# Kernel tuning notes

Measured on AMD Instinct MI355X. Metric: run time of the kernel, lower is better.

The kernel has to match this reference:

```python
import jax, jax.numpy as jnp
import numpy as np

WEIGHT = 0.1
TEMPERATURE = 0.07
EPS_NORM = 1e-12   # F.normalize eps
EPS_DEN = 1e-6     # denominator eps in pos_mask.sum()


def setup_inputs() -> dict:
    key = jax.random.key(0)
    k1, k2 = jax.random.split(key)
    features = jax.random.normal(k1, (4, 1000, 2048), dtype=jnp.float32)
    target = jax.random.randint(k2, (4, 1000), 0, 16, dtype=jnp.int64)
    return {"features": features, "target": target}


def _per_sample_loss(f, t):
    # f: [N, C], t: [N]
    N = f.shape[0]
    # F.normalize(dim=1)
    norm = jnp.maximum(jnp.linalg.norm(f, axis=1, keepdims=True), EPS_NORM)
    f = f / norm
    # [N, N] cosine similarities scaled by temperature
    sim = jnp.matmul(f, f.T) / TEMPERATURE
    eye = jnp.eye(N, dtype=f.dtype)
    pos = (t[:, None] == t[None, :]).astype(f.dtype) * (1.0 - eye)
    neg = 1.0 - pos - eye
    pos_sim = sim * pos
    # -log(exp(pos_sim) / (exp(pos_sim) + sum_j exp(sim)*neg))  summed over ALL entries
    denom = jnp.exp(pos_sim) + jnp.sum(jnp.exp(sim) * neg, axis=1, keepdims=True)
    loss_mat = jnp.log(denom) - pos_sim
    pos_sum = pos.sum()
    return loss_mat.sum() / (pos_sum + EPS_DEN), pos_sum


def reference(features, target):
    # features: [B, N, C] (already 3-D: no subsampling / interpolation paths fire)
    losses, pos_sums = jax.vmap(_per_sample_loss)(features, target)
    valid = pos_sums > 0
    num_pairs = valid.sum().astype(features.dtype)
    total = jnp.where(valid, losses, 0.0).sum()
    return jnp.where(num_pairs > 0, WEIGHT * total / num_pairs,
                     jnp.asarray(WEIGHT * 0.1, dtype=features.dtype))
```

## Files before the change

### kernel.cpp

```cpp
#include <hip/hip_runtime.h>
#include <math.h>

#define BB 4
#define NN 1000
#define NP 1024
#define CC 2048
#define TINV (1.0f / 0.07f)
#define BK 64

#define FNORM_BYTES ((size_t)BB * NP * CC * 2)
#define SIMP_BYTES  ((size_t)2 * BB * NP * NP * 4)
#define RL_BYTES    ((size_t)BB * NP * 4)

typedef __bf16 bf16x8 __attribute__((ext_vector_type(8)));
typedef float  f32x4  __attribute__((ext_vector_type(4)));
typedef float  f32x16 __attribute__((ext_vector_type(16)));

__device__ __forceinline__ void load_lds16(const void* g, void* l) {
    __builtin_amdgcn_global_load_lds(
        (const __attribute__((address_space(1))) unsigned int*)g,
        (__attribute__((address_space(3))) unsigned int*)l, 16, 0, 0);
}

__device__ __forceinline__ float blk_sum(float v, volatile float* lds) {
    int lane = threadIdx.x & 63;
    int wid  = threadIdx.x >> 6;
#pragma unroll
    for (int off = 32; off; off >>= 1) v += __shfl_down(v, off);
    __syncthreads();
    if (lane == 0) lds[wid] = v;
    __syncthreads();
    return lds[0] + lds[1] + lds[2] + lds[3];
}

__device__ __forceinline__ float wave_sum(float v) {
#pragma unroll
    for (int off = 32; off; off >>= 1) v += __shfl_down(v, off);
    return __shfl(v, 0);
}

__global__ __launch_bounds__(256) void norm_bf16_kernel(const float* __restrict__ f,
                                                        __bf16* __restrict__ out) {
    __shared__ float lds[4];
    __shared__ float scale_s;
    const int blk = blockIdx.x;
    const int b = blk >> 10, r = blk & (NP - 1);
    __bf16* dst = out + ((size_t)b * NP + r) * CC;
    const int tid = threadIdx.x;

    if (r >= NN) {
        ((uint4*)dst)[tid] = make_uint4(0u, 0u, 0u, 0u);
        return;
    }
    const float* src = f + ((size_t)b * NN + r) * CC;

    float ss = 0.f;
#pragma unroll
    for (int h = 0; h < 2; ++h) {
        float4 v = ((const float4*)src)[tid + h * 256];
        ss += v.x * v.x + v.y * v.y + v.z * v.z + v.w * v.w;
    }
    float tot = blk_sum(ss, lds);
    if (tid == 0) scale_s = 1.0f / fmaxf(sqrtf(tot), 1e-12f);
    __syncthreads();
    const float sc = scale_s;

    float4 v0 = ((const float4*)src)[tid * 2];
    float4 v1 = ((const float4*)src)[tid * 2 + 1];
    bf16x8 o;
    o[0] = (__bf16)(v0.x * sc); o[1] = (__bf16)(v0.y * sc);
    o[2] = (__bf16)(v0.z * sc); o[3] = (__bf16)(v0.w * sc);
    o[4] = (__bf16)(v1.x * sc); o[5] = (__bf16)(v1.y * sc);
    o[6] = (__bf16)(v1.z * sc); o[7] = (__bf16)(v1.w * sc);
    *(bf16x8*)(dst + tid * 8) = o;
}

__global__ __launch_bounds__(256) void simgemm_mfma(const __bf16* __restrict__ fn,
                                                    float* __restrict__ simp) {
    __shared__ __bf16 As[128 * BK];
    __shared__ __bf16 Bs[128 * BK];

    const int bz = blockIdx.z;
    const int b  = bz >> 1;
    const int kbeg = (bz & 1) * (CC / 2);
    const int tI = blockIdx.y * 128;
    const int tJ = blockIdx.x * 128;
    const __bf16* base = fn + (size_t)b * NP * CC;
    float* S = simp + (size_t)bz * NP * NP;

    const int tid  = threadIdx.x;
    const int wid  = tid >> 6;
    const int lane = tid & 63;
    const int wm   = wid >> 1;
    const int wn   = wid & 1;
    const int ln32 = lane & 31;
    const int kh   = lane >> 5;
    const int sw   = ln32 & 7;

    const int srow   = tid >> 3;
    const int schunk = (tid & 7) ^ (srow & 7);
    const __bf16* gA = base + (size_t)(tI + srow) * CC + kbeg + schunk * 8;
    const __bf16* gB = base + (size_t)(tJ + srow) * CC + kbeg + schunk * 8;
    __bf16* lA = As + (size_t)wid * 8 * BK;
    __bf16* lB = Bs + (size_t)wid * 8 * BK;

    f32x16 acc[2][2] = {};

    for (int k0 = 0; k0 < CC / 2; k0 += BK) {
#pragma unroll
        for (int r = 0; r < 4; ++r)
            load_lds16(gA + k0 + (size_t)r * 32 * CC, lA + r * 32 * BK);
#pragma unroll
        for (int r = 0; r < 4; ++r)
            load_lds16(gB + k0 + (size_t)r * 32 * CC, lB + r * 32 * BK);
        __syncthreads();

#pragma unroll
        for (int kc = 0; kc < 4; ++kc) {
            const int c = kc * 2 + kh;
            const int co = (c ^ sw) * 8;
            bf16x8 a0 = *(const bf16x8*)&As[(wm * 64      + ln32) * BK + co];
            bf16x8 a1 = *(const bf16x8*)&As[(wm * 64 + 32 + ln32) * BK + co];
            bf16x8 b0 = *(const bf16x8*)&Bs[(wn * 64      + ln32) * BK + co];
            bf16x8 b1 = *(const bf16x8*)&Bs[(wn * 64 + 32 + ln32) * BK + co];
            acc[0][0] = __builtin_amdgcn_mfma_f32_32x32x16_bf16(a0, b0, acc[0][0], 0, 0, 0);
            acc[0][1] = __builtin_amdgcn_mfma_f32_32x32x16_bf16(a0, b1, acc[0][1], 0, 0, 0);
            acc[1][0] = __builtin_amdgcn_mfma_f32_32x32x16_bf16(a1, b0, acc[1][0], 0, 0, 0);
            acc[1][1] = __builtin_amdgcn_mfma_f32_32x32x16_bf16(a1, b1, acc[1][1], 0, 0, 0);
        }
        __syncthreads();
    }

#pragma unroll
    for (int at = 0; at < 2; ++at) {
#pragma unroll
        for (int bt = 0; bt < 2; ++bt) {
            const int col = tJ + wn * 64 + bt * 32 + ln32;
#pragma unroll
            for (int r = 0; r < 16; ++r) {
                const int row = tI + wm * 64 + at * 32 + (r & 3) + 8 * (r >> 2) + 4 * kh;
                S[(size_t)row * NP + col] = acc[at][bt][r] * TINV;
            }
        }
    }
}

__global__ __launch_bounds__(256) void rowloss_kernel(const float* __restrict__ simp,
                                                      const int* __restrict__ tgt,
                                                      float* __restrict__ rloss,
                                                      float* __restrict__ rpos) {
    __shared__ int ts[NN];
    __shared__ float rowv[4][NP];
    const int b = blockIdx.y;
    const int wid = threadIdx.x >> 6, lane = threadIdx.x & 63;
    const int* t = tgt + (size_t)b * NN;
    for (int j = threadIdx.x; j < NN; j += 256) ts[j] = t[j];
    __syncthreads();

    const int i = blockIdx.x * 4 + wid;
    const float* r0 = simp + (size_t)(2 * b) * NP * NP + (size_t)i * NP;
    const float* r1 = r0 + (size_t)NP * NP;
    const int ti = ts[i];

    float sneg = 0.f, pcnt = 0.f;
    for (int g = lane; g < NN / 4; g += 64) {
        float4 a = ((const float4*)r0)[g];
        float4 c = ((const float4*)r1)[g];
        float4 v = make_float4(a.x + c.x, a.y + c.y, a.z + c.z, a.w + c.w);
        *(float4*)&rowv[wid][g * 4] = v;
        int4 tj = *(const int4*)&ts[g * 4];
        const int j = g * 4;
        if (j + 0 != i) { if (tj.x == ti) pcnt += 1.f; else sneg += __expf(v.x); }
        if (j + 1 != i) { if (tj.y == ti) pcnt += 1.f; else sneg += __expf(v.y); }
        if (j + 2 != i) { if (tj.z == ti) pcnt += 1.f; else sneg += __expf(v.z); }
        if (j + 3 != i) { if (tj.w == ti) pcnt += 1.f; else sneg += __expf(v.w); }
    }
    const float Sv = wave_sum(sneg);
    const float p  = wave_sum(pcnt);

    float term = 0.f;
    for (int g = lane; g < NN / 4; g += 64) {
        float4 v = *(const float4*)&rowv[wid][g * 4];
        int4 tj = *(const int4*)&ts[g * 4];
        const int j = g * 4;
        if (j + 0 != i && tj.x == ti) term += __logf(__expf(v.x) + Sv) - v.x;
        if (j + 1 != i && tj.y == ti) term += __logf(__expf(v.y) + Sv) - v.y;
        if (j + 2 != i && tj.z == ti) term += __logf(__expf(v.z) + Sv) - v.z;
        if (j + 3 != i && tj.w == ti) term += __logf(__expf(v.w) + Sv) - v.w;
    }
    const float tt = wave_sum(term);
    if (lane == 0) {
        rloss[b * NP + i] = tt + ((float)NN - p) * __logf(1.f + Sv);
        rpos [b * NP + i] = p;
    }
}

__global__ __launch_bounds__(256) void final_kernel(const float* __restrict__ rloss,
                                                    const float* __restrict__ rpos,
                                                    float* __restrict__ out) {
    __shared__ float lds[4];
    float total = 0.f, np = 0.f;
    for (int b = 0; b < BB; ++b) {
        float l = 0.f, p = 0.f;
        for (int i = threadIdx.x; i < NN; i += 256) {
            l += rloss[b * NP + i];
            p += rpos [b * NP + i];
        }
        float ls = blk_sum(l, lds);
        float ps = blk_sum(p, lds);
        if (ps > 0.f) { total += ls / (ps + 1e-6f); np += 1.f; }
    }
    if (threadIdx.x == 0)
        out[0] = (np > 0.f) ? 0.1f * total / np : 0.1f * 0.1f;
}

extern "C" void kernel_launch(void* const* d_in, const int* in_sizes, int n_in,
                              void* d_out, int out_size, void* d_ws, size_t ws_size,
                              hipStream_t stream) {
    const float* feat = (const float*)d_in[0];
    const int*   tgt  = (const int*)d_in[1];
    __bf16* fnorm = (__bf16*)d_ws;
    float*  simp  = (float*)((char*)d_ws + FNORM_BYTES);
    float*  rloss = (float*)((char*)d_ws + FNORM_BYTES + SIMP_BYTES);
    float*  rpos  = (float*)((char*)d_ws + FNORM_BYTES + SIMP_BYTES + RL_BYTES);

    norm_bf16_kernel<<<dim3(BB * NP), 256, 0, stream>>>(feat, fnorm);
    simgemm_mfma<<<dim3(NP / 128, NP / 128, 2 * BB), 256, 0, stream>>>(fnorm, simp);
    rowloss_kernel<<<dim3(NN / 4, BB), 256, 0, stream>>>(simp, tgt, rloss, rpos);
    final_kernel<<<1, 256, 0, stream>>>(rloss, rpos, (float*)d_out);
}
```

Before: 120.5 us.

## Store split-K similarity partials in bf16 and double-buffer GEMM LDS tiles

The split-K similarity partials are now written and read as bf16 instead of fp32. This halves the global-memory traffic between the GEMM and the row-loss kernel, and the row-loss loop now loads 8 bf16 values per lane. The GEMM main loop also gets two LDS buffers, so the next K-tile's global-to-LDS loads are issued before the current tile is computed. The cost is precision: scaled similarities can reach about 14, and rounding each partial to bf16 before exponentiation may push the loss past tolerance.

After: 116.1 us. 1.04x faster.

```diff
diff --git a/kernel.cpp b/kernel.cpp
--- a/kernel.cpp
+++ b/kernel.cpp
@@ -9,7 +9,7 @@
 #define BK 64
 
 #define FNORM_BYTES ((size_t)BB * NP * CC * 2)
-#define SIMP_BYTES  ((size_t)2 * BB * NP * NP * 4)
+#define SIMB_BYTES  ((size_t)2 * BB * NP * NP * 2)
 #define RL_BYTES    ((size_t)BB * NP * 4)
 
 typedef __bf16 bf16x8 __attribute__((ext_vector_type(8)));
@@ -76,9 +76,9 @@
 }
 
 __global__ __launch_bounds__(256) void simgemm_mfma(const __bf16* __restrict__ fn,
-                                                    float* __restrict__ simp) {
-    __shared__ __bf16 As[128 * BK];
-    __shared__ __bf16 Bs[128 * BK];
+                                                    __bf16* __restrict__ simb) {
+    __shared__ __bf16 As0[128 * BK], As1[128 * BK];
+    __shared__ __bf16 Bs0[128 * BK], Bs1[128 * BK];
 
     const int bz = blockIdx.z;
     const int b  = bz >> 1;
@@ -86,7 +86,7 @@
     const int tI = blockIdx.y * 128;
     const int tJ = blockIdx.x * 128;
     const __bf16* base = fn + (size_t)b * NP * CC;
-    float* S = simp + (size_t)bz * NP * NP;
+    __bf16* S = simb + (size_t)bz * NP * NP;
 
     const int tid  = threadIdx.x;
     const int wid  = tid >> 6;
@@ -101,35 +101,48 @@
     const int schunk = (tid & 7) ^ (srow & 7);
     const __bf16* gA = base + (size_t)(tI + srow) * CC + kbeg + schunk * 8;
     const __bf16* gB = base + (size_t)(tJ + srow) * CC + kbeg + schunk * 8;
-    __bf16* lA = As + (size_t)wid * 8 * BK;
-    __bf16* lB = Bs + (size_t)wid * 8 * BK;
+    const int wvoff = wid * 8 * BK;
 
     f32x16 acc[2][2] = {};
 
-    for (int k0 = 0; k0 < CC / 2; k0 += BK) {
-#pragma unroll
-        for (int r = 0; r < 4; ++r)
-            load_lds16(gA + k0 + (size_t)r * 32 * CC, lA + r * 32 * BK);
-#pragma unroll
-        for (int r = 0; r < 4; ++r)
-            load_lds16(gB + k0 + (size_t)r * 32 * CC, lB + r * 32 * BK);
+#define STAGE(k0, A, B)                                                      \
+    {                                                                        \
+        _Pragma("unroll")                                                    \
+        for (int r = 0; r < 4; ++r)                                          \
+            load_lds16(gA + (k0) + (size_t)r * 32 * CC, (A) + r * 32 * BK + wvoff); \
+        _Pragma("unroll")                                                    \
+        for (int r = 0; r < 4; ++r)                                          \
+            load_lds16(gB + (k0) + (size_t)r * 32 * CC, (B) + r * 32 * BK + wvoff); \
+    }
+
+#define COMPUTE(A, B)                                                        \
+    {                                                                        \
+        _Pragma("unroll")                                                    \
+        for (int kc = 0; kc < 4; ++kc) {                                     \
+            const int co = ((kc * 2 + kh) ^ sw) * 8;                         \
+            bf16x8 a0 = *(const bf16x8*)&(A)[(wm * 64      + ln32) * BK + co]; \
+            bf16x8 a1 = *(const bf16x8*)&(A)[(wm * 64 + 32 + ln32) * BK + co]; \
+            bf16x8 b0 = *(const bf16x8*)&(B)[(wn * 64      + ln32) * BK + co]; \
+            bf16x8 b1 = *(const bf16x8*)&(B)[(wn * 64 + 32 + ln32) * BK + co]; \
+            acc[0][0] = __builtin_amdgcn_mfma_f32_32x32x16_bf16(a0, b0, acc[0][0], 0, 0, 0); \
+            acc[0][1] = __builtin_amdgcn_mfma_f32_32x32x16_bf16(a0, b1, acc[0][1], 0, 0, 0); \
+            acc[1][0] = __builtin_amdgcn_mfma_f32_32x32x16_bf16(a1, b0, acc[1][0], 0, 0, 0); \
+            acc[1][1] = __builtin_amdgcn_mfma_f32_32x32x16_bf16(a1, b1, acc[1][1], 0, 0, 0); \
+        }                                                                    \
+    }
+
+    STAGE(0, As0, Bs0);
+#pragma unroll 1
+    for (int k0 = 0; k0 < CC / 2; k0 += 2 * BK) {
         __syncthreads();
-
-#pragma unroll
-        for (int kc = 0; kc < 4; ++kc) {
-            const int c = kc * 2 + kh;
-            const int co = (c ^ sw) * 8;
-            bf16x8 a0 = *(const bf16x8*)&As[(wm * 64      + ln32) * BK + co];
-            bf16x8 a1 = *(const bf16x8*)&As[(wm * 64 + 32 + ln32) * BK + co];
-            bf16x8 b0 = *(const bf16x8*)&Bs[(wn * 64      + ln32) * BK + co];
-            bf16x8 b1 = *(const bf16x8*)&Bs[(wn * 64 + 32 + ln32) * BK + co];
-            acc[0][0] = __builtin_amdgcn_mfma_f32_32x32x16_bf16(a0, b0, acc[0][0], 0, 0, 0);
-            acc[0][1] = __builtin_amdgcn_mfma_f32_32x32x16_bf16(a0, b1, acc[0][1], 0, 0, 0);
-            acc[1][0] = __builtin_amdgcn_mfma_f32_32x32x16_bf16(a1, b0, acc[1][0], 0, 0, 0);
-            acc[1][1] = __builtin_amdgcn_mfma_f32_32x32x16_bf16(a1, b1, acc[1][1], 0, 0, 0);
-        }
+        if (k0 + BK < CC / 2) STAGE(k0 + BK, As1, Bs1);
+        COMPUTE(As0, Bs0);
         __syncthreads();
-    }
+        if (k0 + 2 * BK < CC / 2) STAGE(k0 + 2 * BK, As0, Bs0);
+        COMPUTE(As1, Bs1);
+    }
+#undef STAGE
+#undef COMPUTE
 
 #pragma unroll
     for (int at = 0; at < 2; ++at) {
@@ -139,17 +152,17 @@
 #pragma unroll
             for (int r = 0; r < 16; ++r) {
                 const int row = tI + wm * 64 + at * 32 + (r & 3) + 8 * (r >> 2) + 4 * kh;
-                S[(size_t)row * NP + col] = acc[at][bt][r] * TINV;
+                S[(size_t)row * NP + col] = (__bf16)(acc[at][bt][r] * TINV);
             }
         }
     }
 }
 
-__global__ __launch_bounds__(256) void rowloss_kernel(const float* __restrict__ simp,
+__global__ __launch_bounds__(256) void rowloss_kernel(const __bf16* __restrict__ simb,
                                                       const int* __restrict__ tgt,
                                                       float* __restrict__ rloss,
                                                       float* __restrict__ rpos) {
-    __shared__ int ts[NN];
+    __shared__ __align__(16) int ts[NN];
     __shared__ float rowv[4][NP];
     const int b = blockIdx.y;
     const int wid = threadIdx.x >> 6, lane = threadIdx.x & 63;
@@ -158,35 +171,44 @@
     __syncthreads();
 
     const int i = blockIdx.x * 4 + wid;
-    const float* r0 = simp + (size_t)(2 * b) * NP * NP + (size_t)i * NP;
-    const float* r1 = r0 + (size_t)NP * NP;
+    const __bf16* r0 = simb + (size_t)(2 * b) * NP * NP + (size_t)i * NP;
+    const __bf16* r1 = r0 + (size_t)NP * NP;
     const int ti = ts[i];
 
     float sneg = 0.f, pcnt = 0.f;
-    for (int g = lane; g < NN / 4; g += 64) {
-        float4 a = ((const float4*)r0)[g];
-        float4 c = ((const float4*)r1)[g];
-        float4 v = make_float4(a.x + c.x, a.y + c.y, a.z + c.z, a.w + c.w);
-        *(float4*)&rowv[wid][g * 4] = v;
-        int4 tj = *(const int4*)&ts[g * 4];
-        const int j = g * 4;
-        if (j + 0 != i) { if (tj.x == ti) pcnt += 1.f; else sneg += __expf(v.x); }
-        if (j + 1 != i) { if (tj.y == ti) pcnt += 1.f; else sneg += __expf(v.y); }
-        if (j + 2 != i) { if (tj.z == ti) pcnt += 1.f; else sneg += __expf(v.z); }
-        if (j + 3 != i) { if (tj.w == ti) pcnt += 1.f; else sneg += __expf(v.w); }
+    for (int g = lane; g < NN / 8; g += 64) {
+        bf16x8 va = ((const bf16x8*)r0)[g];
+        bf16x8 vb = ((const bf16x8*)r1)[g];
+        float v[8];
+#pragma unroll
+        for (int k = 0; k < 8; ++k) v[k] = (float)va[k] + (float)vb[k];
+        *(f32x4*)&rowv[wid][g * 8]     = *(f32x4*)&v[0];
+        *(f32x4*)&rowv[wid][g * 8 + 4] = *(f32x4*)&v[4];
+        const int jb = g * 8;
+#pragma unroll
+        for (int k = 0; k < 8; ++k) {
+            const int j = jb + k;
+            if (j != i) {
+                if (ts[j] == ti) pcnt += 1.f;
+                else             sneg += __expf(v[k]);
+            }
+        }
     }
     const float Sv = wave_sum(sneg);
     const float p  = wave_sum(pcnt);
 
     float term = 0.f;
-    for (int g = lane; g < NN / 4; g += 64) {
-        float4 v = *(const float4*)&rowv[wid][g * 4];
-        int4 tj = *(const int4*)&ts[g * 4];
-        const int j = g * 4;
-        if (j + 0 != i && tj.x == ti) term += __logf(__expf(v.x) + Sv) - v.x;
-        if (j + 1 != i && tj.y == ti) term += __logf(__expf(v.y) + Sv) - v.y;
-        if (j + 2 != i && tj.z == ti) term += __logf(__expf(v.z) + Sv) - v.z;
-        if (j + 3 != i && tj.w == ti) term += __logf(__expf(v.w) + Sv) - v.w;
+    for (int g = lane; g < NN / 8; g += 64) {
+        const int jb = g * 8;
+        float v[8];
+        *(f32x4*)&v[0] = *(const f32x4*)&rowv[wid][jb];
+        *(f32x4*)&v[4] = *(const f32x4*)&rowv[wid][jb + 4];
+#pragma unroll
+        for (int k = 0; k < 8; ++k) {
+            const int j = jb + k;
+            if (j != i && ts[j] == ti)
+                term += __logf(__expf(v[k]) + Sv) - v[k];
+        }
     }
     const float tt = wave_sum(term);
     if (lane == 0) {
@@ -219,13 +241,14 @@
                               hipStream_t stream) {
     const float* feat = (const float*)d_in[0];
     const int*   tgt  = (const int*)d_in[1];
-    __bf16* fnorm = (__bf16*)d_ws;
-    float*  simp  = (float*)((char*)d_ws + FNORM_BYTES);
-    float*  rloss = (float*)((char*)d_ws + FNORM_BYTES + SIMP_BYTES);
-    float*  rpos  = (float*)((char*)d_ws + FNORM_BYTES + SIMP_BYTES + RL_BYTES);
+    char* ws = (char*)d_ws;
+    __bf16* fnorm = (__bf16*)ws;                  ws += FNORM_BYTES;
+    __bf16* simb  = (__bf16*)ws;                  ws += SIMB_BYTES;
+    float*  rloss = (float*)ws;                   ws += RL_BYTES;
+    float*  rpos  = (float*)ws;
 
     norm_bf16_kernel<<<dim3(BB * NP), 256, 0, stream>>>(feat, fnorm);
-    simgemm_mfma<<<dim3(NP / 128, NP / 128, 2 * BB), 256, 0, stream>>>(fnorm, simp);
-    rowloss_kernel<<<dim3(NN / 4, BB), 256, 0, stream>>>(simp, tgt, rloss, rpos);
+    simgemm_mfma<<<dim3(NP / 128, NP / 128, 2 * BB), 256, 0, stream>>>(fnorm, simb);
+    rowloss_kernel<<<dim3(NN / 4, BB), 256, 0, stream>>>(simb, tgt, rloss, rpos);
     final_kernel<<<1, 256, 0, stream>>>(rloss, rpos, (float*)d_out);
 }
```
